# Optimization experiments

Hardware: AMD Instinct MI355X
Metric: run time of the kernel (lower is better)

The kernel has to match this reference:

```python
import jax, jax.numpy as jnp
import numpy as np

EPSILON = 1e-8
NUM_STEPS = 1000
S_OFFSET = 0.0001
POWER = 2
CLIPMAX = 0.999
B = 1048576


def _schedule():
    t = jnp.arange(0, NUM_STEPS + 1, dtype=jnp.float32)
    f_t = jnp.cos(np.pi / 2 * (t / NUM_STEPS + S_OFFSET) / (1 + S_OFFSET)) ** POWER
    alpha_bars = f_t / f_t[0]
    betas = jnp.concatenate([jnp.zeros([1], jnp.float32), 1.0 - alpha_bars[1:] / alpha_bars[:-1]])
    betas = jnp.minimum(betas, CLIPMAX)
    sigmas = jnp.sqrt(betas[1:] * ((1.0 - alpha_bars[:-1]) / (1.0 - alpha_bars[1:])))
    sigmas = jnp.concatenate([jnp.zeros([1], jnp.float32), sigmas])
    return alpha_bars, betas, sigmas


def setup_inputs() -> dict:
    key = jax.random.key(0)
    k1, k2, k3, k4, k5 = jax.random.split(key, 5)
    lt = jax.random.normal(k1, (B, 6), dtype=jnp.float32)
    predicted_l0 = jax.random.normal(k2, (B, 6), dtype=jnp.float32)
    pred_lattice = jax.random.normal(k3, (B, 3, 3), dtype=jnp.float32)
    z_noise = jax.random.normal(k4, (B, 6), dtype=jnp.float32)  # torch.randn_like(lt), frozen
    t = jax.random.randint(k5, (B,), 0, NUM_STEPS, dtype=jnp.int64)
    alpha_bars, betas, sigmas = _schedule()
    return {
        "lt": lt,
        "predicted_l0": predicted_l0,
        "pred_lattice": pred_lattice,
        "alpha_bars": alpha_bars,
        "betas": betas,
        "sigmas": sigmas,
        "z_noise": z_noise,
        "t": t,
    }


def reference(lt, predicted_l0, pred_lattice, alpha_bars, betas, sigmas, z_noise, t):
    # VP_lattice.reverse
    alpha = 1.0 - betas[t]
    alpha = jnp.maximum(alpha, 1.0 - betas[-2])  # clamp_min
    alpha_bar = alpha_bars[t]
    sigma = sigmas[t][:, None]

    # polar_decomposition: only the symmetric factor L_tilda = V diag(S) V^T is used
    _, S, Vt = jnp.linalg.svd(pred_lattice, full_matrices=False)  # (B,3),(B,3,3)
    L = jnp.einsum("bji,bj,bjk->bik", Vt, S, Vt)  # Vt^T @ diag(S) @ Vt
    L = (L + jnp.swapaxes(L, 1, 2)) / 2  # symmetrize

    # symmetric_matrix_to_vector: upper triangular incl. diagonal
    vec = jnp.stack([L[:, 0, 0], L[:, 0, 1], L[:, 0, 2], L[:, 1, 1], L[:, 1, 2], L[:, 2, 2]], axis=1)

    predicted_noise = lt - (vec + predicted_l0) / 2
    z = jnp.where((t > 1)[:, None], z_noise, jnp.zeros_like(z_noise))
    coef = (1.0 / jnp.sqrt(alpha + EPSILON))[:, None]
    scale = ((1.0 - alpha) / jnp.sqrt(1.0 - alpha_bar + EPSILON))[:, None]
    return coef * (lt - scale * predicted_noise) + sigma * z
```

## Files before the change

### kernel.cpp

```cpp
#include <hip/hip_runtime.h>


#define NUM_STEPS 1000
#define TBL 1008
#define BLOCK 256
#define WAVES 4
#define TILES 2
#define RPB (BLOCK * TILES)

#define W_PLAT 0
#define W_LT   576
#define W_PL0  960
#define W_ZN   1344
#define W_SZ   1728

__global__ __launch_bounds__(256) void sched_kernel(
    const float* __restrict__ alpha_bars,
    const float* __restrict__ betas,
    const float* __restrict__ sigmas,
    float* __restrict__ ws)
{
    int j = blockIdx.x * blockDim.x + threadIdx.x;
    if (j >= TBL) return;
    if (j <= NUM_STEPS) {
        float beta_last = betas[NUM_STEPS - 1];
        float alpha = 1.0f - fminf(betas[j], beta_last);
        float coef  = 1.0f / sqrtf(alpha + 1e-8f);
        float scale = (1.0f - alpha) / sqrtf(1.0f - alpha_bars[j] + 1e-8f);
        ws[j]           = coef * (1.0f - scale);
        ws[TBL + j]     = 0.5f * coef * scale;
        ws[2 * TBL + j] = (j > 1) ? sigmas[j] : 0.0f;
    } else {
        ws[j] = 0.0f; ws[TBL + j] = 0.0f; ws[2 * TBL + j] = 0.0f;
    }
}

__device__ __forceinline__ void sqrtm_vec(const float* __restrict__ pr,
                                          float vv[6])
{
    float a00 = pr[0], a01 = pr[1], a02 = pr[2];
    float a10 = pr[3], a11 = pr[4], a12 = pr[5];
    float a20 = pr[6], a21 = pr[7], a22 = pr[8];

    float m00 = a00*a00 + a10*a10 + a20*a20;
    float m01 = a00*a01 + a10*a11 + a20*a21;
    float m02 = a00*a02 + a10*a12 + a20*a22;
    float m11 = a01*a01 + a11*a11 + a21*a21;
    float m12 = a01*a02 + a11*a12 + a21*a22;
    float m22 = a02*a02 + a12*a12 + a22*a22;

    float q  = (m00 + m11 + m22) * (1.0f/3.0f);
    float b00 = m00 - q, b11 = m11 - q, b22 = m22 - q;
    float p1 = m01*m01 + m02*m02 + m12*m12;
    float p2 = b00*b00 + b11*b11 + b22*b22 + 2.0f*p1;
    float p  = sqrtf(p2 * (1.0f/6.0f));
    float detB = b00*(b11*b22 - m12*m12)
               - m01*(m01*b22 - m12*m02)
               + m02*(m01*m12 - b11*m02);
    float pinv = __fdividef(1.0f, fmaxf(p, 1e-20f));
    float r = 0.5f * detB * pinv * pinv * pinv;
    r = fminf(fmaxf(r, -1.0f), 1.0f);

    float ar = fabsf(r);
    float sq = sqrtf(1.0f - ar);
    float pl = 1.5707288f + ar * (-0.2121144f + ar * (0.0742610f - ar * 0.0187293f));
    float ac = sq * pl;
    float acr = (r >= 0.0f) ? ac : (3.14159265358979f - ac);
    float phi = acr * (1.0f/3.0f);
    float mu1 = q + 2.0f*p*__cosf(phi);
    float mu3 = q + 2.0f*p*__cosf(phi + 2.0943951023931953f);
    float mu2 = 3.0f*q - mu1 - mu3;
    float l1 = sqrtf(fmaxf(mu1, 0.0f));
    float l2 = sqrtf(fmaxf(mu2, 0.0f));
    float l3 = sqrtf(fmaxf(mu3, 0.0f));

    float IU   = l1 + l2 + l3;
    float IIU  = l1*(l2 + l3) + l2*l3;
    float IIIU = l1*l2*l3;
    float denom = (l1 + l2) * (l1 + l3) * (l2 + l3);
    float dinv  = __fdividef(1.0f, fmaxf(denom, 1e-25f));
    float sd = (IU*IU - IIU) * dinv;
    float td = IU * IIIU * dinv;
    float nd = -dinv;

    float mm00 = m00*m00 + m01*m01 + m02*m02;
    float mm01 = m00*m01 + m01*m11 + m02*m12;
    float mm02 = m00*m02 + m01*m12 + m02*m22;
    float mm11 = m01*m01 + m11*m11 + m12*m12;
    float mm12 = m01*m02 + m11*m12 + m12*m22;
    float mm22 = m02*m02 + m12*m12 + m22*m22;

    vv[0] = nd*mm00 + sd*m00 + td;
    vv[1] = nd*mm01 + sd*m01;
    vv[2] = nd*mm02 + sd*m02;
    vv[3] = nd*mm11 + sd*m11 + td;
    vv[4] = nd*mm12 + sd*m12;
    vv[5] = nd*mm22 + sd*m22 + td;
}

__global__ __launch_bounds__(BLOCK) void vp_lattice_kernel(
    const float* __restrict__ lt,
    const float* __restrict__ pl0,
    const float* __restrict__ plat,
    const float* __restrict__ alpha_bars,
    const float* __restrict__ betas,
    const float* __restrict__ sigmas,
    const float* __restrict__ z_noise,
    const int*   __restrict__ t,
    float* __restrict__ out,
    int n,
    const float* __restrict__ ws,
    int use_ws)
{
    __shared__ __align__(16) float sA[TBL];
    __shared__ __align__(16) float sB[TBL];
    __shared__ __align__(16) float sS[TBL];
    __shared__ __align__(16) float sW[WAVES * W_SZ];

    const int tid  = threadIdx.x;
    const int lane = tid & 63;
    const int wv   = tid >> 6;
    const int rowBase = blockIdx.x * RPB;

    if (use_ws) {
        const float4* w4 = reinterpret_cast<const float4*>(ws);
        float4* a4 = reinterpret_cast<float4*>(sA);
        float4* b4 = reinterpret_cast<float4*>(sB);
        float4* s4 = reinterpret_cast<float4*>(sS);
        for (int j = tid; j < TBL / 4; j += BLOCK) {
            a4[j] = w4[j];
            b4[j] = w4[TBL / 4 + j];
            s4[j] = w4[2 * (TBL / 4) + j];
        }
    } else {
        float beta_last = betas[NUM_STEPS - 1];
        for (int j = tid; j < TBL; j += BLOCK) {
            float A = 0.0f, Bc = 0.0f, S = 0.0f;
            if (j <= NUM_STEPS) {
                float alpha = 1.0f - fminf(betas[j], beta_last);
                float coef  = 1.0f / sqrtf(alpha + 1e-8f);
                float scale = (1.0f - alpha) / sqrtf(1.0f - alpha_bars[j] + 1e-8f);
                A  = coef * (1.0f - scale);
                Bc = 0.5f * coef * scale;
                S  = (j > 1) ? sigmas[j] : 0.0f;
            }
            sA[j] = A; sB[j] = Bc; sS[j] = S;
        }
    }
    __syncthreads();

    float* w = sW + wv * W_SZ;

#pragma unroll
    for (int tile = 0; tile < TILES; ++tile) {
        const int rowW = rowBase + tile * BLOCK + wv * 64;

        if (rowW + 64 <= n) {
            const float* gP = plat    + (size_t)rowW * 9;
            const float* gL = lt      + (size_t)rowW * 6;
            const float* gQ = pl0     + (size_t)rowW * 6;
            const float* gZ = z_noise + (size_t)rowW * 6;

            float4 pA = reinterpret_cast<const float4*>(gP)[lane];
            float4 pB = reinterpret_cast<const float4*>(gP)[64 + lane];
            float  pC = gP[512 + lane];
            float4 lA = reinterpret_cast<const float4*>(gL)[lane];
            float2 lB = reinterpret_cast<const float2*>(gL + 256)[lane];
            float4 qA = reinterpret_cast<const float4*>(gQ)[lane];
            float2 qB = reinterpret_cast<const float2*>(gQ + 256)[lane];
            float4 zA = reinterpret_cast<const float4*>(gZ)[lane];
            float2 zB = reinterpret_cast<const float2*>(gZ + 256)[lane];
            int ti = t[rowW + lane];

            reinterpret_cast<float4*>(w + W_PLAT)[lane]      = pA;
            reinterpret_cast<float4*>(w + W_PLAT)[64 + lane] = pB;
            w[W_PLAT + 512 + lane]                           = pC;
            reinterpret_cast<float4*>(w + W_LT)[lane]        = lA;
            reinterpret_cast<float2*>(w + W_LT + 256)[lane]  = lB;
            reinterpret_cast<float4*>(w + W_PL0)[lane]       = qA;
            reinterpret_cast<float2*>(w + W_PL0 + 256)[lane] = qB;
            reinterpret_cast<float4*>(w + W_ZN)[lane]        = zA;
            reinterpret_cast<float2*>(w + W_ZN + 256)[lane]  = zB;

            float va[6];
            sqrtm_vec(w + W_PLAT + lane * 9, va);

            float A  = sA[ti];
            float Bc = sB[ti];
            float S  = sS[ti];

            const float* lr = w + W_LT  + lane * 6;
            const float* qr = w + W_PL0 + lane * 6;
            const float* zr = w + W_ZN  + lane * 6;

            float o[6];
#pragma unroll
            for (int c = 0; c < 6; ++c) {
                float lc = lr[c];
                o[c] = A * lc + Bc * (va[c] + qr[c]) + S * zr[c];
            }

            float2* ow = reinterpret_cast<float2*>(w + W_PLAT);
            ow[lane * 3 + 0] = make_float2(o[0], o[1]);
            ow[lane * 3 + 1] = make_float2(o[2], o[3]);
            ow[lane * 3 + 2] = make_float2(o[4], o[5]);

            float* oG = out + (size_t)rowW * 6;
            reinterpret_cast<float4*>(oG)[lane] =
                reinterpret_cast<const float4*>(w + W_PLAT)[lane];
            reinterpret_cast<float2*>(oG + 256)[lane] =
                reinterpret_cast<const float2*>(w + W_PLAT + 256)[lane];
        } else {
            int row = rowW + lane;
            if (row < n) {
                float ab[9];
#pragma unroll
                for (int k = 0; k < 9; ++k) ab[k] = plat[(size_t)row * 9 + k];
                float va[6];
                sqrtm_vec(ab, va);
                int ti = t[row];
                float A  = sA[ti];
                float Bc = sB[ti];
                float S  = sS[ti];
                size_t b6 = (size_t)row * 6;
#pragma unroll
                for (int c = 0; c < 6; ++c) {
                    float lc = lt[b6 + c];
                    out[b6 + c] = A * lc + Bc * (va[c] + pl0[b6 + c]) + S * z_noise[b6 + c];
                }
            }
        }
    }
}

extern "C" void kernel_launch(void* const* d_in, const int* in_sizes, int n_in,
                              void* d_out, int out_size, void* d_ws, size_t ws_size,
                              hipStream_t stream) {
    const float* lt         = (const float*)d_in[0];
    const float* pl0        = (const float*)d_in[1];
    const float* plat       = (const float*)d_in[2];
    const float* alpha_bars = (const float*)d_in[3];
    const float* betas      = (const float*)d_in[4];
    const float* sigmas     = (const float*)d_in[5];
    const float* z_noise    = (const float*)d_in[6];
    const int*   t          = (const int*)d_in[7];
    float* out = (float*)d_out;
    float* ws  = (float*)d_ws;

    int n = in_sizes[0] / 6;
    int use_ws = (ws != nullptr && ws_size >= (size_t)(3 * TBL * sizeof(float)));

    if (use_ws) {
        sched_kernel<<<(TBL + 255) / 256, 256, 0, stream>>>(alpha_bars, betas, sigmas, ws);
    }
    int grid = (n + RPB - 1) / RPB;
    vp_lattice_kernel<<<grid, BLOCK, 0, stream>>>(
        lt, pl0, plat, alpha_bars, betas, sigmas, z_noise, t, out, n, ws, use_ws);
}
```

Baseline: 157.0 us.

## Stage inputs via direct global-to-LDS DMA and fetch coefficients as packed float4 from global

Replaces register-staged coalesced loads with global_load_lds DMA instructions that copy each wave's plat, lt, pl0, z_noise and t slices straight into LDS. The schedule table becomes one packed float4 per step read from global/L2 instead of being copied into shared memory by every block. Blocks drop to one tile of 256 rows, with no __syncthreads and less LDS per block. Output is now written directly as float2 per lane instead of being restaged through LDS, which may coalesce less well.

```diff
diff --git a/kernel.cpp b/kernel.cpp
--- a/kernel.cpp
+++ b/kernel.cpp
@@ -1,42 +1,50 @@
 #include <hip/hip_runtime.h>
+#include <stdint.h>
 
 
 #define NUM_STEPS 1000
 #define TBL 1008
 #define BLOCK 256
 #define WAVES 4
-#define TILES 2
-#define RPB (BLOCK * TILES)
+#define RPB 256
 
 #define W_PLAT 0
 #define W_LT   576
 #define W_PL0  960
 #define W_ZN   1344
-#define W_SZ   1728
+#define W_T    1728
+#define W_SZF  1792
+#define W_SZB  7168
+
+#define AS1 __attribute__((address_space(1)))
+#define AS3 __attribute__((address_space(3)))
+
+__device__ __forceinline__ void dma16(const void* g, void* s) {
+    __builtin_amdgcn_global_load_lds((const AS1 void*)g, (AS3 void*)s, 16, 0, 0);
+}
 
 __global__ __launch_bounds__(256) void sched_kernel(
     const float* __restrict__ alpha_bars,
     const float* __restrict__ betas,
     const float* __restrict__ sigmas,
-    float* __restrict__ ws)
+    float4* __restrict__ ws)
 {
     int j = blockIdx.x * blockDim.x + threadIdx.x;
     if (j >= TBL) return;
+    float4 v = make_float4(0.f, 0.f, 0.f, 0.f);
     if (j <= NUM_STEPS) {
         float beta_last = betas[NUM_STEPS - 1];
         float alpha = 1.0f - fminf(betas[j], beta_last);
         float coef  = 1.0f / sqrtf(alpha + 1e-8f);
         float scale = (1.0f - alpha) / sqrtf(1.0f - alpha_bars[j] + 1e-8f);
-        ws[j]           = coef * (1.0f - scale);
-        ws[TBL + j]     = 0.5f * coef * scale;
-        ws[2 * TBL + j] = (j > 1) ? sigmas[j] : 0.0f;
-    } else {
-        ws[j] = 0.0f; ws[TBL + j] = 0.0f; ws[2 * TBL + j] = 0.0f;
+        v.x = coef * (1.0f - scale);
+        v.y = 0.5f * coef * scale;
+        v.z = (j > 1) ? sigmas[j] : 0.0f;
     }
-}
-
-__device__ __forceinline__ void sqrtm_vec(const float* __restrict__ pr,
-                                          float vv[6])
+    ws[j] = v;
+}
+
+__device__ __forceinline__ void sqrtm_vec(const float* pr, float vv[6])
 {
     float a00 = pr[0], a01 = pr[1], a02 = pr[2];
     float a10 = pr[3], a11 = pr[4], a12 = pr[5];
@@ -109,126 +117,100 @@
     const int*   __restrict__ t,
     float* __restrict__ out,
     int n,
-    const float* __restrict__ ws,
+    const float4* __restrict__ coefs,
     int use_ws)
 {
-    __shared__ __align__(16) float sA[TBL];
-    __shared__ __align__(16) float sB[TBL];
-    __shared__ __align__(16) float sS[TBL];
-    __shared__ __align__(16) float sW[WAVES * W_SZ];
+    __shared__ __align__(16) float sW[WAVES * W_SZF];
 
     const int tid  = threadIdx.x;
     const int lane = tid & 63;
     const int wv   = tid >> 6;
-    const int rowBase = blockIdx.x * RPB;
-
-    if (use_ws) {
-        const float4* w4 = reinterpret_cast<const float4*>(ws);
-        float4* a4 = reinterpret_cast<float4*>(sA);
-        float4* b4 = reinterpret_cast<float4*>(sB);
-        float4* s4 = reinterpret_cast<float4*>(sS);
-        for (int j = tid; j < TBL / 4; j += BLOCK) {
-            a4[j] = w4[j];
-            b4[j] = w4[TBL / 4 + j];
-            s4[j] = w4[2 * (TBL / 4) + j];
-        }
+    const int rowW = blockIdx.x * RPB + wv * 64;
+
+    float* w = sW + wv * W_SZF;
+
+    if (rowW + 64 <= n) {
+        const char* pP = (const char*)(plat    + (size_t)rowW * 9);
+        const char* pL = (const char*)(lt      + (size_t)rowW * 6);
+        const char* pQ = (const char*)(pl0     + (size_t)rowW * 6);
+        const char* pZ = (const char*)(z_noise + (size_t)rowW * 6);
+        const char* pT = (const char*)(t + rowW);
+        char* wb = (char*)w;
+        const int lb = lane * 16;
+
+        dma16(pP + lb,        wb       );
+        dma16(pP + 1024 + lb, wb + 1024);
+        { int s = 2048 + lb;
+          dma16((s < 2304) ? pP + s : pL + (s - 2304), wb + 2048); }
+        { int s = 3072 + lb;
+          dma16((s < 3840) ? pL + (s - 2304) : pQ + (s - 3840), wb + 3072); }
+        dma16(pQ + 256 + lb,  wb + 4096);
+        { int s = 5120 + lb;
+          dma16((s < 5376) ? pQ + (s - 3840) : pZ + (s - 5376), wb + 5120); }
+        { int s = 6144 + lb;
+          dma16((s < 6912) ? pZ + (s - 5376) : pT + (s - 6912), wb + 6144); }
+
+        asm volatile("s_waitcnt vmcnt(0)" ::: "memory");
+        __builtin_amdgcn_sched_barrier(0);
+
+        int ti = reinterpret_cast<const int*>(w + W_T)[lane];
+        float4 cf;
+        if (use_ws) {
+            cf = coefs[ti];
+        } else {
+            float beta_last = betas[NUM_STEPS - 1];
+            float alpha = 1.0f - fminf(betas[ti], beta_last);
+            float coef  = 1.0f / sqrtf(alpha + 1e-8f);
+            float scale = (1.0f - alpha) / sqrtf(1.0f - alpha_bars[ti] + 1e-8f);
+            cf.x = coef * (1.0f - scale);
+            cf.y = 0.5f * coef * scale;
+            cf.z = (ti > 1) ? sigmas[ti] : 0.0f;
+        }
+
+        float va[6];
+        sqrtm_vec(w + W_PLAT + lane * 9, va);
+
+        const float* lr = w + W_LT  + lane * 6;
+        const float* qr = w + W_PL0 + lane * 6;
+        const float* zr = w + W_ZN  + lane * 6;
+
+        float o[6];
+#pragma unroll
+        for (int c = 0; c < 6; ++c) {
+            float lc = lr[c];
+            o[c] = cf.x * lc + cf.y * (va[c] + qr[c]) + cf.z * zr[c];
+        }
+
+        float* oG = out + (size_t)(rowW + lane) * 6;
+        reinterpret_cast<float2*>(oG)[0] = make_float2(o[0], o[1]);
+        reinterpret_cast<float2*>(oG)[1] = make_float2(o[2], o[3]);
+        reinterpret_cast<float2*>(oG)[2] = make_float2(o[4], o[5]);
     } else {
-        float beta_last = betas[NUM_STEPS - 1];
-        for (int j = tid; j < TBL; j += BLOCK) {
-            float A = 0.0f, Bc = 0.0f, S = 0.0f;
-            if (j <= NUM_STEPS) {
-                float alpha = 1.0f - fminf(betas[j], beta_last);
-                float coef  = 1.0f / sqrtf(alpha + 1e-8f);
-                float scale = (1.0f - alpha) / sqrtf(1.0f - alpha_bars[j] + 1e-8f);
-                A  = coef * (1.0f - scale);
-                Bc = 0.5f * coef * scale;
-                S  = (j > 1) ? sigmas[j] : 0.0f;
-            }
-            sA[j] = A; sB[j] = Bc; sS[j] = S;
-        }
-    }
-    __syncthreads();
-
-    float* w = sW + wv * W_SZ;
-
+        int row = rowW + lane;
+        if (row >= n) return;
+        float ab[9];
 #pragma unroll
-    for (int tile = 0; tile < TILES; ++tile) {
-        const int rowW = rowBase + tile * BLOCK + wv * 64;
-
-        if (rowW + 64 <= n) {
-            const float* gP = plat    + (size_t)rowW * 9;
-            const float* gL = lt      + (size_t)rowW * 6;
-            const float* gQ = pl0     + (size_t)rowW * 6;
-            const float* gZ = z_noise + (size_t)rowW * 6;
-
-            float4 pA = reinterpret_cast<const float4*>(gP)[lane];
-            float4 pB = reinterpret_cast<const float4*>(gP)[64 + lane];
-            float  pC = gP[512 + lane];
-            float4 lA = reinterpret_cast<const float4*>(gL)[lane];
-            float2 lB = reinterpret_cast<const float2*>(gL + 256)[lane];
-            float4 qA = reinterpret_cast<const float4*>(gQ)[lane];
-            float2 qB = reinterpret_cast<const float2*>(gQ + 256)[lane];
-            float4 zA = reinterpret_cast<const float4*>(gZ)[lane];
-            float2 zB = reinterpret_cast<const float2*>(gZ + 256)[lane];
-            int ti = t[rowW + lane];
-
-            reinterpret_cast<float4*>(w + W_PLAT)[lane]      = pA;
-            reinterpret_cast<float4*>(w + W_PLAT)[64 + lane] = pB;
-            w[W_PLAT + 512 + lane]                           = pC;
-            reinterpret_cast<float4*>(w + W_LT)[lane]        = lA;
-            reinterpret_cast<float2*>(w + W_LT + 256)[lane]  = lB;
-            reinterpret_cast<float4*>(w + W_PL0)[lane]       = qA;
-            reinterpret_cast<float2*>(w + W_PL0 + 256)[lane] = qB;
-            reinterpret_cast<float4*>(w + W_ZN)[lane]        = zA;
-            reinterpret_cast<float2*>(w + W_ZN + 256)[lane]  = zB;
-
-            float va[6];
-            sqrtm_vec(w + W_PLAT + lane * 9, va);
-
-            float A  = sA[ti];
-            float Bc = sB[ti];
-            float S  = sS[ti];
-
-            const float* lr = w + W_LT  + lane * 6;
-            const float* qr = w + W_PL0 + lane * 6;
-            const float* zr = w + W_ZN  + lane * 6;
-
-            float o[6];
+        for (int k = 0; k < 9; ++k) ab[k] = plat[(size_t)row * 9 + k];
+        float va[6];
+        sqrtm_vec(ab, va);
+        int ti = t[row];
+        float4 cf;
+        if (use_ws) {
+            cf = coefs[ti];
+        } else {
+            float beta_last = betas[NUM_STEPS - 1];
+            float alpha = 1.0f - fminf(betas[ti], beta_last);
+            float coef  = 1.0f / sqrtf(alpha + 1e-8f);
+            float scale = (1.0f - alpha) / sqrtf(1.0f - alpha_bars[ti] + 1e-8f);
+            cf.x = coef * (1.0f - scale);
+            cf.y = 0.5f * coef * scale;
+            cf.z = (ti > 1) ? sigmas[ti] : 0.0f;
+        }
+        size_t b6 = (size_t)row * 6;
 #pragma unroll
-            for (int c = 0; c < 6; ++c) {
-                float lc = lr[c];
-                o[c] = A * lc + Bc * (va[c] + qr[c]) + S * zr[c];
-            }
-
-            float2* ow = reinterpret_cast<float2*>(w + W_PLAT);
-            ow[lane * 3 + 0] = make_float2(o[0], o[1]);
-            ow[lane * 3 + 1] = make_float2(o[2], o[3]);
-            ow[lane * 3 + 2] = make_float2(o[4], o[5]);
-
-            float* oG = out + (size_t)rowW * 6;
-            reinterpret_cast<float4*>(oG)[lane] =
-                reinterpret_cast<const float4*>(w + W_PLAT)[lane];
-            reinterpret_cast<float2*>(oG + 256)[lane] =
-                reinterpret_cast<const float2*>(w + W_PLAT + 256)[lane];
-        } else {
-            int row = rowW + lane;
-            if (row < n) {
-                float ab[9];
-#pragma unroll
-                for (int k = 0; k < 9; ++k) ab[k] = plat[(size_t)row * 9 + k];
-                float va[6];
-                sqrtm_vec(ab, va);
-                int ti = t[row];
-                float A  = sA[ti];
-                float Bc = sB[ti];
-                float S  = sS[ti];
-                size_t b6 = (size_t)row * 6;
-#pragma unroll
-                for (int c = 0; c < 6; ++c) {
-                    float lc = lt[b6 + c];
-                    out[b6 + c] = A * lc + Bc * (va[c] + pl0[b6 + c]) + S * z_noise[b6 + c];
-                }
-            }
+        for (int c = 0; c < 6; ++c) {
+            float lc = lt[b6 + c];
+            out[b6 + c] = cf.x * lc + cf.y * (va[c] + pl0[b6 + c]) + cf.z * z_noise[b6 + c];
         }
     }
 }
@@ -245,10 +227,10 @@
     const float* z_noise    = (const float*)d_in[6];
     const int*   t          = (const int*)d_in[7];
     float* out = (float*)d_out;
-    float* ws  = (float*)d_ws;
+    float4* ws = (float4*)d_ws;
 
     int n = in_sizes[0] / 6;
-    int use_ws = (ws != nullptr && ws_size >= (size_t)(3 * TBL * sizeof(float)));
+    int use_ws = (ws != nullptr && ws_size >= (size_t)(TBL * sizeof(float4)));
 
     if (use_ws) {
         sched_kernel<<<(TBL + 255) / 256, 256, 0, stream>>>(alpha_bars, betas, sigmas, ws);
```

After: 153.3 us. -2.4%, faster.
